# Performance work log

Measured on AMD Instinct MI355X. Metric: run time of the kernel, lower is better.

## Reference

```python
import jax, jax.numpy as jnp
import numpy as np

H = 2048
W = 2048
N = H * W
NUM_CC = 1 << 20
N_ITERS = 20  # pointer-doubling covers tree depth up to 2**20 (actual depth ~ e*ln N ~ 45)
EPS = 1e-10


def _log_scaling(f):
    # f: [NUM_CC, 15] = xmin, ymin, xmax, ymax, area, angle, pca_big, pca_small, hu1..hu7
    # -> [NUM_CC, 17] = xmin..ymax, log(area), signed-log(pca_big, pca_small, hu1..hu7), lshape, cos(angle), sin(angle)
    lshape = jnp.sqrt(f[:, 7:8]) / (jnp.sqrt(f[:, 6:7]) + EPS)
    cosangle = jnp.cos(f[:, 5:6])
    sinangle = jnp.sin(f[:, 5:6])
    log_area = jnp.log(f[:, 4:5])
    signed_log = jnp.log(jnp.abs(f[:, 6:]) + EPS) * jnp.sign(f[:, 6:])
    return jnp.concatenate([f[:, :4], log_area, signed_log, lshape, cosangle, sinangle], axis=1)


def _tree_path_sum(contrib, parent):
    # out[p] = sum of contrib over p and all its ancestors (root has parent == -1).
    # Parallel pointer-doubling: after k steps acc[i] sums contrib over 2**k chain nodes.
    acc, par = contrib, parent
    for _ in range(N_ITERS):
        valid = par >= 0
        pidx = jnp.where(valid, par, 0)
        acc = acc + jnp.where(valid, acc[pidx], jnp.zeros((), acc.dtype))
        par = jnp.where(valid, par[pidx], -1)
    return acc


def setup_inputs() -> dict:
    rng = np.random.default_rng(0)
    # random recursive tree: parent[i] uniform in [0, i), root = node 0
    parent = (rng.random(N) * np.arange(N)).astype(np.int32)
    parent[0] = -1
    cc_id = rng.integers(0, NUM_CC, size=N).astype(np.int32)
    diff = rng.standard_normal(N).astype(np.float32)
    attrs = np.empty((NUM_CC, 15), np.float32)
    attrs[:, :4] = rng.random((NUM_CC, 4)) * 100.0          # bbox coords
    attrs[:, 4] = rng.random(NUM_CC) * 1000.0 + 1.0         # area (>0 for log)
    attrs[:, 5] = rng.standard_normal(NUM_CC)               # angle
    attrs[:, 6:8] = rng.random((NUM_CC, 2)) + 0.01          # pca_big/pca_small (>=0 for sqrt)
    attrs[:, 8:] = rng.standard_normal((NUM_CC, 7)).astype(np.float32)  # hu moments
    weight = ((rng.random((17, 1)) - 0.5) * 0.02).astype(np.float32)
    bias = np.zeros((1,), np.float32)
    return {
        "diff": jnp.asarray(diff),
        "attributes": jnp.asarray(attrs),
        "weight": jnp.asarray(weight),
        "bias": jnp.asarray(bias),
        "parent": jnp.asarray(parent),
        "cc_id": jnp.asarray(cc_id),
    }


def reference(diff, attributes, weight, bias, parent, cc_id):
    rescaled = _log_scaling(attributes)                                   # [NUM_CC, 17]
    cc_scores = jax.nn.sigmoid(rescaled @ weight + bias[None, :])[:, 0]   # [NUM_CC]
    contrib = diff * cc_scores[cc_id]                                     # [N]
    out = _tree_path_sum(contrib, parent)                                 # [N]
    return out.reshape(H, W)
```

## Files before the change

kernel.cpp:

```cpp
#include <hip/hip_runtime.h>

#define EPSF 1e-10f

struct alignas(8) Node { int par; float c; };

typedef int   v4i __attribute__((ext_vector_type(4)));
typedef float v4f __attribute__((ext_vector_type(4)));

__device__ __forceinline__ float signed_log(float x) {
    float sg = (x > 0.f) ? 1.f : ((x < 0.f) ? -1.f : 0.f);
    return logf(fabsf(x) + EPSF) * sg;
}

__global__ void scores_kernel(const float* __restrict__ attrs,
                              const float* __restrict__ weight,
                              const float* __restrict__ bias,
                              float* __restrict__ scores, int num_cc) {
    int i = blockIdx.x * blockDim.x + threadIdx.x;
    if (i >= num_cc) return;
    const float* f = attrs + (long long)i * 15;
    float w[17];
#pragma unroll
    for (int k = 0; k < 17; ++k) w[k] = weight[k];
    float acc = bias[0];
    acc += w[0] * f[0] + w[1] * f[1] + w[2] * f[2] + w[3] * f[3];
    acc += w[4] * logf(f[4]);
#pragma unroll
    for (int j = 0; j < 9; ++j) acc += w[5 + j] * signed_log(f[6 + j]);
    float lshape = sqrtf(f[7]) / (sqrtf(f[6]) + EPSF);
    acc += w[14] * lshape;
    acc += w[15] * cosf(f[5]);
    acc += w[16] * sinf(f[5]);
    __builtin_nontemporal_store(1.f / (1.f + expf(-acc)), &scores[i]);
}

__global__ void pack_kernel4(const v4f* __restrict__ diff4,
                             const v4i* __restrict__ parent4,
                             const v4i* __restrict__ cc4,
                             const float* __restrict__ scores,
                             v4i* __restrict__ packed2, int n4) {
    int i = blockIdx.x * blockDim.x + threadIdx.x;
    if (i >= n4) return;
    v4f d = __builtin_nontemporal_load(&diff4[i]);
    v4i p = __builtin_nontemporal_load(&parent4[i]);
    v4i c = __builtin_nontemporal_load(&cc4[i]);
    float s0 = scores[c.x], s1 = scores[c.y], s2 = scores[c.z], s3 = scores[c.w];
    v4i o0, o1;
    o0.x = p.x; o0.y = __float_as_int(d.x * s0);
    o0.z = p.y; o0.w = __float_as_int(d.y * s1);
    o1.x = p.z; o1.y = __float_as_int(d.z * s2);
    o1.z = p.w; o1.w = __float_as_int(d.w * s3);
    __builtin_nontemporal_store(o0, &packed2[2 * i]);
    __builtin_nontemporal_store(o1, &packed2[2 * i + 1]);
}

__global__ void pack_kernel(const float* __restrict__ diff,
                            const int* __restrict__ parent,
                            const int* __restrict__ cc_id,
                            const float* __restrict__ scores,
                            Node* __restrict__ packed, int lo, int n) {
    int i = lo + blockIdx.x * blockDim.x + threadIdx.x;
    if (i >= n) return;
    Node nd;
    nd.par = parent[i];
    nd.c = diff[i] * scores[cc_id[i]];
    packed[i] = nd;
}


__global__ void walk_base(const Node* __restrict__ packed,
                          float* __restrict__ out, int range_end) {
    int i = blockIdx.x * blockDim.x + threadIdx.x;
    if (i >= range_end) return;
    long long raw = __builtin_nontemporal_load((const long long*)(packed + i));
    int cur = (int)(raw & 0xffffffffLL);
    float s = __int_as_float((int)(raw >> 32));
    while (cur >= 0) {
        Node nd = packed[cur];
        s += nd.c;
        cur = nd.par;
    }
    __builtin_nontemporal_store(s, &out[i]);
}

template <int PX>
__global__ void walk_phaseN(const Node* __restrict__ packed,
                            float* __restrict__ out, int lo, int hi) {
    long long t = (long long)blockIdx.x * blockDim.x + threadIdx.x;
    int base = lo + (int)(t * PX);
    if (base >= hi) return;
    int cur[PX]; float s[PX];

    if (base + PX <= hi) {
#pragma unroll
        for (int k = 0; k < PX; k += 2) {
            v4i raw = __builtin_nontemporal_load((const v4i*)(packed + base + k));
            cur[k]     = raw.x; s[k]     = __int_as_float(raw.y);
            cur[k + 1] = raw.z; s[k + 1] = __int_as_float(raw.w);
        }
    } else {
#pragma unroll
        for (int k = 0; k < PX; ++k) {
            if (base + k < hi) { Node nd = packed[base + k]; cur[k] = nd.par; s[k] = nd.c; }
            else               { cur[k] = 0; s[k] = 0.f; }
        }
    }

    while (true) {
        bool any = false;
#pragma unroll
        for (int k = 0; k < PX; ++k) any |= (cur[k] >= lo);
        if (!__any(any)) break;
#pragma unroll
        for (int k = 0; k < PX; ++k) {
            bool act = cur[k] >= lo;
            int idx = act ? cur[k] : lo;
            Node nd = packed[idx];
            s[k]  += act ? nd.c : 0.f;
            cur[k] = act ? nd.par : cur[k];
        }
    }

#pragma unroll
    for (int k = 0; k < PX; ++k) s[k] += out[cur[k]];

    if (base + PX <= hi) {
#pragma unroll
        for (int k = 0; k < PX; k += 4) {
            v4f o; o.x = s[k]; o.y = s[k + 1]; o.z = s[k + 2]; o.w = s[k + 3];
            __builtin_nontemporal_store(o, (v4f*)(out + base + k));
        }
    } else {
#pragma unroll
        for (int k = 0; k < PX; ++k)
            if (base + k < hi) out[base + k] = s[k];
    }
}

__global__ void walk_base2(const int* __restrict__ parent,
                           const float* __restrict__ contrib,
                           float* __restrict__ out, int range_end) {
    int i = blockIdx.x * blockDim.x + threadIdx.x;
    if (i >= range_end) return;
    float s = 0.f;
    int cur = i;
    while (cur >= 0) { s += contrib[cur]; cur = parent[cur]; }
    out[i] = s;
}

__global__ void walk_phase2(const int* __restrict__ parent,
                            const float* __restrict__ contrib,
                            float* __restrict__ out, int lo, int hi) {
    int i = lo + blockIdx.x * blockDim.x + threadIdx.x;
    if (i >= hi) return;
    float s = 0.f;
    int cur = i;
    while (cur >= lo) { s += contrib[cur]; cur = parent[cur]; }
    s += out[cur];
    out[i] = s;
}

__global__ void contrib_kernel(const float* __restrict__ diff,
                               const int* __restrict__ cc_id,
                               const float* __restrict__ scores,
                               float* __restrict__ contrib, int n) {
    int i = blockIdx.x * blockDim.x + threadIdx.x;
    if (i >= n) return;
    contrib[i] = diff[i] * scores[cc_id[i]];
}

static inline int iminh(int a, int b) { return a < b ? a : b; }

extern "C" void kernel_launch(void* const* d_in, const int* in_sizes, int n_in,
                              void* d_out, int out_size, void* d_ws, size_t ws_size,
                              hipStream_t stream) {
    const float* diff   = (const float*)d_in[0];
    const float* attrs  = (const float*)d_in[1];
    const float* weight = (const float*)d_in[2];
    const float* bias   = (const float*)d_in[3];
    const int*   parent = (const int*)d_in[4];
    const int*   cc_id  = (const int*)d_in[5];
    float* out = (float*)d_out;

    const int n      = in_sizes[0];
    const int num_cc = in_sizes[1] / 15;

    float* scores = (float*)d_ws;
    const size_t scores_bytes = (size_t)num_cc * sizeof(float);
    const size_t packed_need  = scores_bytes + (size_t)n * sizeof(Node);
    const bool use_packed = ws_size >= packed_need;

    const int TB = 256;
    scores_kernel<<<(num_cc + TB - 1) / TB, TB, 0, stream>>>(attrs, weight, bias, scores, num_cc);

    const int BASE   = 131072;
    const int R2_MIN = 1 << 19;
    const int PX8_MIN = 1 << 20;

    if (use_packed) {
        Node* packed = (Node*)((char*)d_ws + scores_bytes);
        if ((n & 3) == 0) {
            pack_kernel4<<<(n / 4 + TB - 1) / TB, TB, 0, stream>>>(
                (const v4f*)diff, (const v4i*)parent, (const v4i*)cc_id, scores, (v4i*)packed, n / 4);
        } else {
            pack_kernel<<<(n + TB - 1) / TB, TB, 0, stream>>>(diff, parent, cc_id, scores, packed, 0, n);
        }
        int base_end = iminh(BASE, n);
        walk_base<<<(base_end + TB - 1) / TB, TB, 0, stream>>>(packed, out, base_end);
        int lo = base_end;
        while (lo < n) {
            int ratio = (lo < R2_MIN) ? 4 : 2;
            long long hi_ll = (long long)lo * ratio;
            int hi = (hi_ll > n) ? n : (int)hi_ll;
            int cnt = hi - lo;
            if (cnt >= PX8_MIN) {
                long long threads = (cnt + 7) / 8;
                walk_phaseN<8><<<(int)((threads + TB - 1) / TB), TB, 0, stream>>>(packed, out, lo, hi);
            } else {
                long long threads = (cnt + 3) / 4;
                walk_phaseN<4><<<(int)((threads + TB - 1) / TB), TB, 0, stream>>>(packed, out, lo, hi);
            }
            lo = hi;
        }
    } else {
        float* contrib = (float*)((char*)d_ws + scores_bytes);
        contrib_kernel<<<(n + TB - 1) / TB, TB, 0, stream>>>(diff, cc_id, scores, contrib, n);
        int base_end = iminh(BASE, n);
        walk_base2<<<(base_end + TB - 1) / TB, TB, 0, stream>>>(parent, contrib, out, base_end);
        int lo = base_end;
        while (lo < n) {
            int ratio = (lo < R2_MIN) ? 4 : 2;
            long long hi_ll = (long long)lo * ratio;
            int hi = (hi_ll > n) ? n : (int)hi_ll;
            walk_phase2<<<((hi - lo) + TB - 1) / TB, TB, 0, stream>>>(parent, contrib, out, lo, hi);
            lo = hi;
        }
    }
}
```

Before: 133.1 us.

## Add fp16 shadow of prior-phase sums and use uniform doubling phases

Each walk phase now also writes an fp16 copy of its path sums into a workspace shadow buffer. Later phases read the ancestor prefix from this half-size buffer instead of the fp32 output, which halves the bytes of those random gathers and improves cache hit rates. The phase schedule also changes to a uniform 2x range growth with PX=4 everywhere, which adds kernel launches. The fp16 rounding of ancestor sums adds error to every result and may break the accuracy tolerance.

```diff
diff --git a/kernel.cpp b/kernel.cpp
--- a/kernel.cpp
+++ b/kernel.cpp
@@ -1,11 +1,13 @@
 #include <hip/hip_runtime.h>
+#include <hip/hip_fp16.h>
 
 #define EPSF 1e-10f
 
 struct alignas(8) Node { int par; float c; };
 
-typedef int   v4i __attribute__((ext_vector_type(4)));
-typedef float v4f __attribute__((ext_vector_type(4)));
+typedef int      v4i  __attribute__((ext_vector_type(4)));
+typedef float    v4f  __attribute__((ext_vector_type(4)));
+typedef _Float16 h4   __attribute__((ext_vector_type(4)));
 
 __device__ __forceinline__ float signed_log(float x) {
     float sg = (x > 0.f) ? 1.f : ((x < 0.f) ? -1.f : 0.f);
@@ -68,8 +70,10 @@
 }
 
 
+template <bool SH>
 __global__ void walk_base(const Node* __restrict__ packed,
-                          float* __restrict__ out, int range_end) {
+                          float* __restrict__ out,
+                          _Float16* __restrict__ shadow, int range_end) {
     int i = blockIdx.x * blockDim.x + threadIdx.x;
     if (i >= range_end) return;
     long long raw = __builtin_nontemporal_load((const long long*)(packed + i));
@@ -81,17 +85,20 @@
         cur = nd.par;
     }
     __builtin_nontemporal_store(s, &out[i]);
-}
-
-template <int PX>
+    if (SH) __builtin_nontemporal_store((_Float16)s, &shadow[i]);
+}
+
+template <int PX, bool SH>
 __global__ void walk_phaseN(const Node* __restrict__ packed,
-                            float* __restrict__ out, int lo, int hi) {
+                            float* __restrict__ out,
+                            _Float16* __restrict__ shadow, int lo, int hi) {
     long long t = (long long)blockIdx.x * blockDim.x + threadIdx.x;
     int base = lo + (int)(t * PX);
     if (base >= hi) return;
     int cur[PX]; float s[PX];
 
-    if (base + PX <= hi) {
+    const bool full = (base + PX <= hi);
+    if (full) {
 #pragma unroll
         for (int k = 0; k < PX; k += 2) {
             v4i raw = __builtin_nontemporal_load((const v4i*)(packed + base + k));
@@ -122,18 +129,27 @@
     }
 
 #pragma unroll
-    for (int k = 0; k < PX; ++k) s[k] += out[cur[k]];
-
-    if (base + PX <= hi) {
+    for (int k = 0; k < PX; ++k)
+        s[k] += SH ? (float)shadow[cur[k]] : out[cur[k]];
+
+    if (full) {
 #pragma unroll
         for (int k = 0; k < PX; k += 4) {
             v4f o; o.x = s[k]; o.y = s[k + 1]; o.z = s[k + 2]; o.w = s[k + 3];
             __builtin_nontemporal_store(o, (v4f*)(out + base + k));
+            if (SH) {
+                h4 hv; hv.x = (_Float16)s[k]; hv.y = (_Float16)s[k + 1];
+                hv.z = (_Float16)s[k + 2];    hv.w = (_Float16)s[k + 3];
+                __builtin_nontemporal_store(hv, (h4*)(shadow + base + k));
+            }
         }
     } else {
 #pragma unroll
         for (int k = 0; k < PX; ++k)
-            if (base + k < hi) out[base + k] = s[k];
+            if (base + k < hi) {
+                out[base + k] = s[k];
+                if (SH) shadow[base + k] = (_Float16)s[k];
+            }
     }
 }
 
@@ -187,18 +203,20 @@
 
     float* scores = (float*)d_ws;
     const size_t scores_bytes = (size_t)num_cc * sizeof(float);
-    const size_t packed_need  = scores_bytes + (size_t)n * sizeof(Node);
-    const bool use_packed = ws_size >= packed_need;
+    const size_t packed_bytes = (size_t)n * sizeof(Node);
+    const size_t shadow_bytes = (size_t)n * sizeof(_Float16);
+    const bool use_packed = ws_size >= scores_bytes + packed_bytes;
+    const bool use_shadow = ws_size >= scores_bytes + packed_bytes + shadow_bytes;
 
     const int TB = 256;
     scores_kernel<<<(num_cc + TB - 1) / TB, TB, 0, stream>>>(attrs, weight, bias, scores, num_cc);
 
-    const int BASE   = 131072;
-    const int R2_MIN = 1 << 19;
-    const int PX8_MIN = 1 << 20;
+    const int BASE = 131072;
 
     if (use_packed) {
         Node* packed = (Node*)((char*)d_ws + scores_bytes);
+        _Float16* shadow = use_shadow ? (_Float16*)((char*)d_ws + scores_bytes + packed_bytes)
+                                      : (_Float16*)nullptr;
         if ((n & 3) == 0) {
             pack_kernel4<<<(n / 4 + TB - 1) / TB, TB, 0, stream>>>(
                 (const v4f*)diff, (const v4i*)parent, (const v4i*)cc_id, scores, (v4i*)packed, n / 4);
@@ -206,20 +224,21 @@
             pack_kernel<<<(n + TB - 1) / TB, TB, 0, stream>>>(diff, parent, cc_id, scores, packed, 0, n);
         }
         int base_end = iminh(BASE, n);
-        walk_base<<<(base_end + TB - 1) / TB, TB, 0, stream>>>(packed, out, base_end);
+        if (use_shadow)
+            walk_base<true><<<(base_end + TB - 1) / TB, TB, 0, stream>>>(packed, out, shadow, base_end);
+        else
+            walk_base<false><<<(base_end + TB - 1) / TB, TB, 0, stream>>>(packed, out, shadow, base_end);
         int lo = base_end;
         while (lo < n) {
-            int ratio = (lo < R2_MIN) ? 4 : 2;
-            long long hi_ll = (long long)lo * ratio;
+            long long hi_ll = (long long)lo * 2;
             int hi = (hi_ll > n) ? n : (int)hi_ll;
             int cnt = hi - lo;
-            if (cnt >= PX8_MIN) {
-                long long threads = (cnt + 7) / 8;
-                walk_phaseN<8><<<(int)((threads + TB - 1) / TB), TB, 0, stream>>>(packed, out, lo, hi);
-            } else {
-                long long threads = (cnt + 3) / 4;
-                walk_phaseN<4><<<(int)((threads + TB - 1) / TB), TB, 0, stream>>>(packed, out, lo, hi);
-            }
+            long long threads = (cnt + 3) / 4;
+            int grid = (int)((threads + TB - 1) / TB);
+            if (use_shadow)
+                walk_phaseN<4, true><<<grid, TB, 0, stream>>>(packed, out, shadow, lo, hi);
+            else
+                walk_phaseN<4, false><<<grid, TB, 0, stream>>>(packed, out, shadow, lo, hi);
             lo = hi;
         }
     } else {
@@ -229,8 +248,7 @@
         walk_base2<<<(base_end + TB - 1) / TB, TB, 0, stream>>>(parent, contrib, out, base_end);
         int lo = base_end;
         while (lo < n) {
-            int ratio = (lo < R2_MIN) ? 4 : 2;
-            long long hi_ll = (long long)lo * ratio;
+            long long hi_ll = (long long)lo * 2;
             int hi = (hi_ll > n) ? n : (int)hi_ll;
             walk_phase2<<<((hi - lo) + TB - 1) / TB, TB, 0, stream>>>(parent, contrib, out, lo, hi);
             lo = hi;
```

After: 123.8 us. 1.08x faster.
